# Optimization experiments

Hardware: AMD Instinct MI355X
Metric: run time of the kernel (lower is better)

Reference implementation:

```python
import jax, jax.numpy as jnp
import numpy as np

N = 8192; S = 32; EMB = 256; NH = 8; HD = EMB // NH; NT = 4; K = 2; L = 2; E = 131072
IN_DIMS = [128, 64, 32, 16]; COUNTS = [4096, 2048, 1024, 1024]
BETA = 1.0; TEMPER = 1.0; SLOPE = 0.2; LN_EPS = 1e-5


def setup_inputs() -> dict:
    key = jax.random.key(0)
    ks = iter(jax.random.split(key, 64))
    def nrm(shape, scale=1.0):
        return jax.random.normal(next(ks), shape, jnp.float32) * scale
    inp = {}
    for i, (d, c) in enumerate(zip(IN_DIMS, COUNTS)):
        inp[f"feat{i}"] = nrm((c, d))
        inp[f"Wfc{i}"] = nrm((d, EMB), d ** -0.5)
        inp[f"bfc{i}"] = nrm((EMB,), 0.01)
    inp["type_emb"] = nrm((NT, NT))
    inp["Wgcn"] = nrm((K, EMB, EMB), EMB ** -0.5)
    inp["bgcn"] = nrm((K, EMB), 0.01)
    inp["Wre"] = nrm((K, NT, NT), NT ** -0.5)
    inp["bre"] = nrm((K, NT), 0.01)
    inp["wtre"] = jnp.ones((K, NT), jnp.float32)
    inp["Wl"] = nrm((L, EMB, EMB), EMB ** -0.5)
    inp["Wr"] = nrm((L, EMB, EMB), EMB ** -0.5)
    inp["al"] = nrm((L, HD), HD ** -0.5)
    inp["ar"] = nrm((L, HD), HD ** -0.5)
    inp["Wrs"] = nrm((L, NT, NT * NH), NT ** -0.5)
    inp["Wrt"] = nrm((L, NT, NT * NH), NT ** -0.5)
    inp["Wfin"] = nrm((L, EMB, EMB), EMB ** -0.5)
    inp["ln_g"] = jnp.ones((L, EMB), jnp.float32)
    inp["ln_b"] = jnp.zeros((L, EMB), jnp.float32)
    inp["src"] = jax.random.randint(next(ks), (E,), 0, N)
    inp["dst"] = jax.random.randint(next(ks), (E,), 0, N)
    inp["node_type"] = jnp.concatenate([jnp.full((c,), t, jnp.int32) for t, c in enumerate(COUNTS)])
    inp["seqs"] = jax.random.randint(next(ks), (N, S), 0, N)
    return inp


def _l2n(x):
    return x / jnp.maximum(jnp.linalg.norm(x, axis=1, keepdims=True), 1e-12)


def _ln(x, g, b):
    m = x.mean(-1, keepdims=True)
    v = ((x - m) ** 2).mean(-1, keepdims=True)
    return (x - m) * jax.lax.rsqrt(v + LN_EPS) * g + b


def _agt(h, rh, Wl_, Wr_, al_, ar_, Wrs_, Wrt_, Wfin_, g_, b_):
    B, Sq, _ = h.shape
    fl = (h @ Wl_).reshape(B, Sq, NH, HD).transpose(0, 2, 1, 3)  # [B,NH,S,HD]
    fr = (h @ Wr_).reshape(B, Sq, NH, HD).transpose(0, 2, 1, 3)
    sl = jnp.einsum('bhsd,d->bhs', jax.nn.leaky_relu(fl, SLOPE), al_)
    sr = jnp.einsum('bhsd,d->bhs', jax.nn.leaky_relu(fr, SLOPE), ar_)
    score = sl[:, :, :, None] + sr[:, :, None, :]  # [B,NH,S,S]
    rk = (rh @ Wrs_).reshape(B, Sq, NH, NT).transpose(0, 2, 1, 3)  # [B,NH,S,NT]
    rq = (rh @ Wrt_).reshape(B, Sq, NH, NT).transpose(0, 2, 1, 3)
    score = score + BETA * jnp.einsum('bhir,bhjr->bhij', rk, rq)
    attn = jax.nn.softmax(score / TEMPER, axis=-1)
    ctx = jnp.einsum('bhij,bhjd->bhid', attn, fr)
    h_sa = ctx.transpose(0, 2, 1, 3).reshape(B, Sq, EMB)
    return _ln(h + h_sa @ Wfin_, g_, b_)


def reference(feat0, feat1, feat2, feat3, Wfc0, bfc0, Wfc1, bfc1, Wfc2, bfc2, Wfc3, bfc3,
              type_emb, Wgcn, bgcn, Wre, bre, wtre, Wl, Wr, al, ar, Wrs, Wrt, Wfin, ln_g, ln_b,
              src, dst, node_type, seqs):
    feats = [feat0, feat1, feat2, feat3]
    Wfcs = [Wfc0, Wfc1, Wfc2, Wfc3]
    bfcs = [bfc0, bfc1, bfc2, bfc3]
    gh = jnp.concatenate([f @ W + b for f, W, b in zip(feats, Wfcs, bfcs)], axis=0)  # [N,EMB]
    Nn = gh.shape[0]
    loop = jnp.arange(Nn, dtype=src.dtype)  # self-loops (graph.add_self_loop)
    src_f = jnp.concatenate([src, loop]); dst_f = jnp.concatenate([dst, loop])
    ones = jnp.ones(src_f.shape[0], jnp.float32)
    outdeg = jnp.clip(jax.ops.segment_sum(ones, src_f, num_segments=Nn), 1.0)
    indeg = jnp.clip(jax.ops.segment_sum(ones, dst_f, num_segments=Nn), 1.0)
    n_out = outdeg ** -0.5; n_in = indeg ** -0.5
    ret = [_l2n(gh)]
    R = type_emb[node_type]  # [N,NT]
    for k in range(K):
        # GraphConv, norm='both', relu
        x = (gh * n_out[:, None]) @ Wgcn[k]
        gh = jax.nn.relu(jax.ops.segment_sum(x[src_f], dst_f, num_segments=Nn) * n_in[:, None] + bgcn[k])
        # REConv: left norm, weight, per-node type scale, scatter-sum, right norm, bias, relu
        r = ((R * n_out[:, None]) @ Wre[k]) * wtre[k][node_type][:, None]
        R = jax.nn.relu(jax.ops.segment_sum(r[src_f], dst_f, num_segments=Nn) * n_in[:, None] + bre[k])
    h = gh[seqs]   # [N,S,EMB]
    rh = R[seqs]   # [N,S,NT]
    for l in range(L):
        h = _agt(h, rh, Wl[l], Wr[l], al[l], ar[l], Wrs[l], Wrt[l], Wfin[l], ln_g[l], ln_b[l])
        ret.append(_l2n(h[:, 0, :]))
    return jnp.concatenate(ret, axis=1)  # [N, EMB*(1+L)]
```

## Files before the change

kernel.cpp:

```cpp
#include <hip/hip_runtime.h>
#include <hip/hip_bf16.h>
#include <cstdint>
#include <cstddef>

typedef unsigned short ushortT;
typedef unsigned int uintT;

using bf16x8 = __attribute__((ext_vector_type(8))) short;
using f32x4  = __attribute__((ext_vector_type(4))) float;

static constexpr int NN  = 8192;
static constexpr int EE  = 131072;
static constexpr float SLOPE  = 0.2f;
static constexpr float LN_EPS = 1e-5f;

#define DEVI __device__ __forceinline__

DEVI float red32(float v) {
  #pragma unroll
  for (int m = 16; m >= 1; m >>= 1) v += __shfl_xor(v, m, 64);
  return v;
}
DEVI float red64(float v) {
  #pragma unroll
  for (int m = 32; m >= 1; m >>= 1) v += __shfl_xor(v, m, 64);
  return v;
}
DEVI float max32(float v) {
  #pragma unroll
  for (int m = 16; m >= 1; m >>= 1) v = fmaxf(v, __shfl_xor(v, m, 64));
  return v;
}
DEVI float blo(uintT u) { union { uintT i; float f; } c; c.i = u << 16; return c.f; }
DEVI float bhi(uintT u) { union { uintT i; float f; } c; c.i = u & 0xffff0000u; return c.f; }
DEVI float b2f(ushortT u) { union { uintT i; float f; } c; c.i = ((uintT)u) << 16; return c.f; }
DEVI ushortT f2bu(float f) {
  __hip_bfloat16 h = __float2bfloat16(f);
  return *reinterpret_cast<ushortT*>(&h);
}
DEVI void storeC(float* p, float v) { *p = v; }
DEVI void storeC(ushortT* p, float v) { *p = f2bu(v); }

__global__ __launch_bounds__(256) void fc_kernel(
    const float* __restrict__ f0, const float* __restrict__ f1,
    const float* __restrict__ f2, const float* __restrict__ f3,
    const float* __restrict__ w0, const float* __restrict__ w1,
    const float* __restrict__ w2, const float* __restrict__ w3,
    const float* __restrict__ b0, const float* __restrict__ b1,
    const float* __restrict__ b2, const float* __restrict__ b3,
    float* __restrict__ gh, float* __restrict__ out)
{
  const int nb = blockIdx.x * 32;
  const int t  = threadIdx.x;
  int base, D;
  const float *F, *W, *Bv;
  if (nb < 4096)      { base = 0;    D = 128; F = f0; W = w0; Bv = b0; }
  else if (nb < 6144) { base = 4096; D = 64;  F = f1; W = w1; Bv = b1; }
  else if (nb < 7168) { base = 6144; D = 32;  F = f2; W = w2; Bv = b2; }
  else                { base = 7168; D = 16;  F = f3; W = w3; Bv = b3; }

  __shared__ float Fs[32 * 128];
  __shared__ float red[32][4];
  __shared__ float nrm[32];

  const int total = 32 * D;
  for (int i = t; i < total; i += 256) Fs[i] = F[(size_t)(nb - base) * D + i];
  __syncthreads();

  float acc[32];
  #pragma unroll
  for (int r = 0; r < 32; ++r) acc[r] = Bv[t];
  for (int d = 0; d < D; ++d) {
    float w = W[(size_t)d * 256 + t];
    #pragma unroll
    for (int r = 0; r < 32; ++r) acc[r] = fmaf(Fs[r * D + d], w, acc[r]);
  }

  const int lane = t & 63, wid = t >> 6;
  #pragma unroll
  for (int r = 0; r < 32; ++r) {
    float v = acc[r] * acc[r];
    for (int o = 32; o > 0; o >>= 1) v += __shfl_down(v, o, 64);
    if (lane == 0) red[r][wid] = v;
  }
  __syncthreads();
  if (t < 32) {
    float s = red[t][0] + red[t][1] + red[t][2] + red[t][3];
    nrm[t] = 1.0f / fmaxf(sqrtf(s), 1e-12f);
  }
  __syncthreads();
  #pragma unroll
  for (int r = 0; r < 32; ++r) {
    gh[(size_t)(nb + r) * 256 + t]  = acc[r];
    out[(size_t)(nb + r) * 768 + t] = acc[r] * nrm[r];
  }
}

__global__ __launch_bounds__(256) void zero_counts(int* outc, int* inc) {
  int g = blockIdx.x * 256 + threadIdx.x;
  if (g < NN) outc[g] = 0; else inc[g - NN] = 0;
}
__global__ __launch_bounds__(256) void count_deg(const int* __restrict__ src,
                                                 const int* __restrict__ dst,
                                                 int* outc, int* inc) {
  int g = blockIdx.x * 256 + threadIdx.x;
  atomicAdd(&outc[src[g]], 1);
  atomicAdd(&inc[dst[g]], 1);
}
__global__ __launch_bounds__(1024) void scan_kernel(
    const int* __restrict__ inc, const int* __restrict__ outc,
    int* __restrict__ offs, int* __restrict__ cur,
    float* __restrict__ n_out, float* __restrict__ n_in)
{
  __shared__ int sums[1024];
  const int t = threadIdx.x;
  int x[8];
  const int base = t * 8;
  int s = 0;
  #pragma unroll
  for (int i = 0; i < 8; ++i) { int v = inc[base + i] + 1; x[i] = s; s += v; }
  sums[t] = s;
  __syncthreads();
  for (int off = 1; off < 1024; off <<= 1) {
    int a = (t >= off) ? sums[t - off] : 0;
    __syncthreads();
    sums[t] += a;
    __syncthreads();
  }
  const int pre = (t > 0) ? sums[t - 1] : 0;
  #pragma unroll
  for (int i = 0; i < 8; ++i) {
    const int o = pre + x[i];
    offs[base + i] = o;
    cur[base + i]  = o;
    n_in[base + i]  = rsqrtf((float)inc[base + i] + 1.0f);
    n_out[base + i] = rsqrtf((float)outc[base + i] + 1.0f);
  }
  if (t == 1023) offs[NN] = sums[1023];
}
__global__ __launch_bounds__(256) void fill_csr(const int* __restrict__ src,
                                                const int* __restrict__ dst,
                                                int* cur, int* __restrict__ csr) {
  int g = blockIdx.x * 256 + threadIdx.x;
  int s, d;
  if (g < EE) { s = src[g]; d = dst[g]; }
  else        { s = g - EE; d = g - EE; }
  int pos = atomicAdd(&cur[d], 1);
  csr[pos] = s;
}
__global__ __launch_bounds__(256) void init_R(const float* __restrict__ type_emb,
                                              const int* __restrict__ nt,
                                              float* __restrict__ R) {
  int g = blockIdx.x * 256 + threadIdx.x;
  int n = g >> 2, c = g & 3;
  R[g] = type_emb[nt[n] * 4 + c];
}

template<bool ROWSCALE, bool STORE, bool RED, typename CT>
__global__ __launch_bounds__(256) void mfma_gemm_kernel(
    const float* __restrict__ A, const float* __restrict__ W,
    const float* __restrict__ rowscale,
    CT* __restrict__ C, const float* __restrict__ avec,
    float* __restrict__ SSo)
{
  const int m0 = blockIdx.x * 64;
  const int n0 = blockIdx.y * 64;
  const int t = threadIdx.x;
  const int w = t >> 6, l = t & 63;
  const int wr = w >> 1, wc = w & 1;
  const int l15 = l & 15, l16 = l >> 4;

  __shared__ alignas(16) ushortT As[64][72];
  __shared__ alignas(16) ushortT Bs[64][72];

  f32x4 acc[2][2];
  #pragma unroll
  for (int mh = 0; mh < 2; ++mh)
    #pragma unroll
    for (int nh = 0; nh < 2; ++nh)
      #pragma unroll
      for (int r = 0; r < 4; ++r) acc[mh][nh][r] = 0.f;

  for (int k0 = 0; k0 < 256; k0 += 64) {
    #pragma unroll
    for (int rep = 0; rep < 16; ++rep) {
      int flat = rep * 256 + t;
      int r = flat >> 6, k = flat & 63;
      float v = A[(size_t)(m0 + r) * 256 + k0 + k];
      if constexpr (ROWSCALE) v *= rowscale[m0 + r];
      As[r][k] = f2bu(v);
    }
    #pragma unroll
    for (int rep = 0; rep < 16; ++rep) {
      int flat = rep * 256 + t;
      int k = flat >> 6, n = flat & 63;
      Bs[n][k] = f2bu(W[(size_t)(k0 + k) * 256 + n0 + n]);
    }
    __syncthreads();
    #pragma unroll
    for (int ks = 0; ks < 2; ++ks) {
      const int kb = ks * 32 + l16 * 8;
      bf16x8 afr[2], bfr[2];
      #pragma unroll
      for (int mh = 0; mh < 2; ++mh)
        afr[mh] = *reinterpret_cast<const bf16x8*>(&As[wr * 32 + mh * 16 + l15][kb]);
      #pragma unroll
      for (int nh = 0; nh < 2; ++nh)
        bfr[nh] = *reinterpret_cast<const bf16x8*>(&Bs[wc * 32 + nh * 16 + l15][kb]);
      #pragma unroll
      for (int mh = 0; mh < 2; ++mh)
        #pragma unroll
        for (int nh = 0; nh < 2; ++nh)
          acc[mh][nh] = __builtin_amdgcn_mfma_f32_16x16x32_bf16(
              afr[mh], bfr[nh], acc[mh][nh], 0, 0, 0);
    }
    __syncthreads();
  }
  if constexpr (STORE) {
    #pragma unroll
    for (int mh = 0; mh < 2; ++mh)
      #pragma unroll
      for (int nh = 0; nh < 2; ++nh)
        #pragma unroll
        for (int r = 0; r < 4; ++r) {
          const int row = m0 + wr * 32 + mh * 16 + l16 * 4 + r;
          const int col = n0 + wc * 32 + nh * 16 + l15;
          storeC(&C[(size_t)row * 256 + col], acc[mh][nh][r]);
        }
  }
  if constexpr (RED) {
    const float av0 = avec[l15], av1 = avec[16 + l15];
    #pragma unroll
    for (int mh = 0; mh < 2; ++mh)
      #pragma unroll
      for (int r = 0; r < 4; ++r) {
        float s = 0.f;
        {
          float x = acc[mh][0][r];
          s = fmaf(x > 0.f ? x : SLOPE * x, av0, s);
          x = acc[mh][1][r];
          s = fmaf(x > 0.f ? x : SLOPE * x, av1, s);
        }
        #pragma unroll
        for (int m = 8; m >= 1; m >>= 1) s += __shfl_xor(s, m, 64);
        if (l15 == 0) {
          const int row = m0 + wr * 32 + mh * 16 + l16 * 4 + r;
          SSo[(size_t)row * 8 + blockIdx.y * 2 + wc] = s;
        }
      }
  }
}

__global__ __launch_bounds__(256) void mfma_wlwr_kernel(
    const float* __restrict__ A,
    const float* __restrict__ Wl_, const float* __restrict__ Wr_,
    float* __restrict__ GR1,
    const float* __restrict__ al_, const float* __restrict__ ar_,
    float* __restrict__ SL, float* __restrict__ SR)
{
  const int m0 = blockIdx.x * 64;
  const int n0 = blockIdx.y * 64;
  const int t = threadIdx.x;
  const int w = t >> 6, l = t & 63;
  const int wr = w >> 1, wc = w & 1;
  const int l15 = l & 15, l16 = l >> 4;

  __shared__ alignas(16) ushortT As[64][72];
  __shared__ alignas(16) ushortT Bl[64][72];
  __shared__ alignas(16) ushortT Br[64][72];

  f32x4 accl[2][2], accr[2][2];
  #pragma unroll
  for (int mh = 0; mh < 2; ++mh)
    #pragma unroll
    for (int nh = 0; nh < 2; ++nh)
      #pragma unroll
      for (int r = 0; r < 4; ++r) { accl[mh][nh][r] = 0.f; accr[mh][nh][r] = 0.f; }

  for (int k0 = 0; k0 < 256; k0 += 64) {
    #pragma unroll
    for (int rep = 0; rep < 16; ++rep) {
      int flat = rep * 256 + t;
      int r = flat >> 6, k = flat & 63;
      As[r][k] = f2bu(A[(size_t)(m0 + r) * 256 + k0 + k]);
    }
    #pragma unroll
    for (int rep = 0; rep < 16; ++rep) {
      int flat = rep * 256 + t;
      int k = flat >> 6, n = flat & 63;
      Bl[n][k] = f2bu(Wl_[(size_t)(k0 + k) * 256 + n0 + n]);
      Br[n][k] = f2bu(Wr_[(size_t)(k0 + k) * 256 + n0 + n]);
    }
    __syncthreads();
    #pragma unroll
    for (int ks = 0; ks < 2; ++ks) {
      const int kb = ks * 32 + l16 * 8;
      bf16x8 afr[2], blr[2], brr[2];
      #pragma unroll
      for (int mh = 0; mh < 2; ++mh)
        afr[mh] = *reinterpret_cast<const bf16x8*>(&As[wr * 32 + mh * 16 + l15][kb]);
      #pragma unroll
      for (int nh = 0; nh < 2; ++nh) {
        blr[nh] = *reinterpret_cast<const bf16x8*>(&Bl[wc * 32 + nh * 16 + l15][kb]);
        brr[nh] = *reinterpret_cast<const bf16x8*>(&Br[wc * 32 + nh * 16 + l15][kb]);
      }
      #pragma unroll
      for (int mh = 0; mh < 2; ++mh)
        #pragma unroll
        for (int nh = 0; nh < 2; ++nh) {
          accl[mh][nh] = __builtin_amdgcn_mfma_f32_16x16x32_bf16(
              afr[mh], blr[nh], accl[mh][nh], 0, 0, 0);
          accr[mh][nh] = __builtin_amdgcn_mfma_f32_16x16x32_bf16(
              afr[mh], brr[nh], accr[mh][nh], 0, 0, 0);
        }
    }
    __syncthreads();
  }
  #pragma unroll
  for (int mh = 0; mh < 2; ++mh)
    #pragma unroll
    for (int nh = 0; nh < 2; ++nh)
      #pragma unroll
      for (int r = 0; r < 4; ++r) {
        const int row = m0 + wr * 32 + mh * 16 + l16 * 4 + r;
        const int col = n0 + wc * 32 + nh * 16 + l15;
        GR1[(size_t)row * 256 + col] = accr[mh][nh][r];
      }
  const float al0 = al_[l15], al1 = al_[16 + l15];
  const float ar0 = ar_[l15], ar1 = ar_[16 + l15];
  #pragma unroll
  for (int mh = 0; mh < 2; ++mh)
    #pragma unroll
    for (int r = 0; r < 4; ++r) {
      float sl = 0.f, sr = 0.f;
      {
        float x = accl[mh][0][r];
        sl = fmaf(x > 0.f ? x : SLOPE * x, al0, sl);
        x = accl[mh][1][r];
        sl = fmaf(x > 0.f ? x : SLOPE * x, al1, sl);
        x = accr[mh][0][r];
        sr = fmaf(x > 0.f ? x : SLOPE * x, ar0, sr);
        x = accr[mh][1][r];
        sr = fmaf(x > 0.f ? x : SLOPE * x, ar1, sr);
      }
      #pragma unroll
      for (int m = 8; m >= 1; m >>= 1) {
        sl += __shfl_xor(sl, m, 64);
        sr += __shfl_xor(sr, m, 64);
      }
      if (l15 == 0) {
        const int row = m0 + wr * 32 + mh * 16 + l16 * 4 + r;
        SL[(size_t)row * 8 + blockIdx.y * 2 + wc] = sl;
        SR[(size_t)row * 8 + blockIdx.y * 2 + wc] = sr;
      }
    }
}

__global__ __launch_bounds__(256) void agg2_kernel(
    const int* __restrict__ offs, const int* __restrict__ csr,
    const ushortT* __restrict__ X, const float* __restrict__ n_in,
    const float* __restrict__ bias, float* __restrict__ ghn,
    ushortT* __restrict__ ghb)
{
  const int n  = blockIdx.x * 2 + (threadIdx.x >> 7);
  const int tc = threadIdx.x & 127;
  const uintT* X2 = reinterpret_cast<const uintT*>(X);
  const int s0 = offs[n], s1 = offs[n + 1];
  float a0 = 0.f, a1 = 0.f;
  for (int i = s0; i < s1; ++i) {
    const uintT u = X2[(size_t)csr[i] * 128 + tc];
    a0 += blo(u);
    a1 += bhi(u);
  }
  const float ni = n_in[n];
  const float g0 = fmaxf(fmaf(a0, ni, bias[2 * tc]), 0.f);
  const float g1 = fmaxf(fmaf(a1, ni, bias[2 * tc + 1]), 0.f);
  float2 g2; g2.x = g0; g2.y = g1;
  reinterpret_cast<float2*>(ghn)[(size_t)n * 128 + tc] = g2;
  if (ghb)
    reinterpret_cast<uintT*>(ghb)[(size_t)n * 128 + tc] =
        (uintT)f2bu(g0) | ((uintT)f2bu(g1) << 16);
}

__global__ __launch_bounds__(256) void re_proj(
    const float* __restrict__ R, const float* __restrict__ n_out,
    const float* __restrict__ Wre, const float* __restrict__ wtre,
    const int* __restrict__ nt, float* __restrict__ rtmp)
{
  int g = blockIdx.x * 256 + threadIdx.x;
  int n = g >> 2, j = g & 3;
  float s = 0.f;
  #pragma unroll
  for (int c = 0; c < 4; ++c) s += R[n * 4 + c] * Wre[c * 4 + j];
  rtmp[g] = s * n_out[n] * wtre[nt[n]];
}
__global__ __launch_bounds__(256) void re_agg(
    const int* __restrict__ offs, const int* __restrict__ csr,
    const float* __restrict__ rtmp, const float* __restrict__ n_in,
    const float* __restrict__ bre, float* __restrict__ Rn)
{
  int g = blockIdx.x * 256 + threadIdx.x;
  int n = g >> 2, j = g & 3;
  float a = 0.f;
  for (int i = offs[n]; i < offs[n + 1]; ++i) a += rtmp[csr[i] * 4 + j];
  Rn[g] = fmaxf(fmaf(a, n_in[n], bre[j]), 0.f);
}
__global__ __launch_bounds__(256) void rkq_kernel(
    const float* __restrict__ R, const float* __restrict__ Wrs,
    const float* __restrict__ Wrt, float* __restrict__ RKQ)
{
  int g = blockIdx.x * 256 + threadIdx.x;
  int n = g >> 7, c = g & 127;
  int which = c >> 5, cc = c & 31;
  const float* Wp = (which == 0) ? Wrs : (which == 1) ? Wrt
                   : (which == 2) ? (Wrs + 128) : (Wrt + 128);
  float s = 0.f;
  #pragma unroll
  for (int r = 0; r < 4; ++r) s += R[n * 4 + r] * Wp[r * 32 + cc];
  RKQ[g] = s;
}

__global__ __launch_bounds__(256) void vec4_kernel(
    const float* __restrict__ ln_g, const float* __restrict__ ln_b,
    const float* __restrict__ Wr2, float* __restrict__ vecs)
{
  const int which = blockIdx.x, t = threadIdx.x;
  const float* s = (which & 1) ? ln_b : ln_g;
  float a = 0.f;
  for (int k = 0; k < 256; ++k) a = fmaf(s[k], Wr2[(size_t)k * 256 + t], a);
  vecs[which * 256 + t] = a;
}
__global__ __launch_bounds__(256) void wg2i_kernel(
    const float* __restrict__ ln_g, const float* __restrict__ Wr2,
    ushortT* __restrict__ Wg2i)
{
  const int gid = blockIdx.x * 256 + threadIdx.x;
  const int ks  = gid >> 10;
  const int cgl = (gid >> 6) & 15;
  const int l   = gid & 63;
  const int col = cgl * 16 + (l & 15);
  const int kb  = ks * 32 + (l >> 4) * 8;
  ushortT v[8];
  #pragma unroll
  for (int e = 0; e < 8; ++e)
    v[e] = f2bu(ln_g[kb + e] * Wr2[(size_t)(kb + e) * 256 + col]);
  *reinterpret_cast<bf16x8*>(&Wg2i[(size_t)gid * 8]) =
      *reinterpret_cast<const bf16x8*>(v);
}
__global__ __launch_bounds__(256) void wcvt_kernel(
    const float* __restrict__ Wl2, const float* __restrict__ Wfin2,
    ushortT* __restrict__ Wl2b, ushortT* __restrict__ Wf2b)
{
  int g = blockIdx.x * 256 + threadIdx.x;
  if (g < 65536) Wl2b[g] = f2bu(Wl2[g]);
  else { int q = g - 65536; Wf2b[q] = f2bu(Wfin2[q]); }
}

__global__ __launch_bounds__(256) void mega8_kernel(
    const int* __restrict__ seqs,
    const ushortT* __restrict__ ghb,
    const ushortT* __restrict__ GW,
    const float* __restrict__ SLg, const float* __restrict__ SRg,
    const float* __restrict__ RKQ,
    const float* __restrict__ vecs,
    const ushortT* __restrict__ Wg2i,
    const ushortT* __restrict__ Wl2b,
    const ushortT* __restrict__ Wf2b,
    const float* __restrict__ al2, const float* __restrict__ ar2,
    const float* __restrict__ ln_g, const float* __restrict__ ln_b,
    float* __restrict__ out)
{
  __shared__ int idx[32];
  __shared__ alignas(16) ushortT bufA[10240];
  __shared__ alignas(16) ushortT bufB[10240];
  __shared__ float SRs[8][32];
  __shared__ float RQs[32][36];
  __shared__ float rk2s[32];
  __shared__ float part[32][4], partq[32][4];
  __shared__ float mu_s[32], rs_s[32];
  __shared__ float SR2s[8][32];
  __shared__ float sl2s[8];
  __shared__ float scp[8][32];
  __shared__ float h1r0s[256];
  __shared__ float ctx2s[256];
  __shared__ float wred4[4];
  __shared__ float nrm1s;

  const int b = blockIdx.x, t = threadIdx.x;
  const int h8 = t >> 5, lo = t & 31;
  const int w = t >> 6, l = t & 63;
  const int l15 = l & 15, l16 = l >> 4;

  if (t < 32) idx[t] = seqs[b * 32 + t];
  __syncthreads();

  const float sli = SLg[(size_t)idx[lo] * 8 + h8];
  const float rk0 = RKQ[(size_t)idx[lo] * 128 + h8 * 4 + 0];
  const float rk1 = RKQ[(size_t)idx[lo] * 128 + h8 * 4 + 1];
  const float rk2_ = RKQ[(size_t)idx[lo] * 128 + h8 * 4 + 2];
  const float rk3 = RKQ[(size_t)idx[lo] * 128 + h8 * 4 + 3];

  {
    const uintT* GWu = reinterpret_cast<const uintT*>(GW);
    #pragma unroll
    for (int rep = 0; rep < 16; ++rep) {
      int flat = rep * 256 + t;
      int j = flat >> 7, cp = flat & 127;
      const uintT u = GWu[(size_t)idx[j] * 128 + cp];
      const int rA = 2 * cp;
      const int k = (rA >> 3) & 3;
      const int off = (((j >> 3) ^ k) << 3) + (j & 7);
      bufA[rA * 40 + off]       = (ushortT)(u & 0xffffu);
      bufA[(rA + 1) * 40 + off] = (ushortT)(u >> 16);
    }
  }
  SRs[h8][lo] = SRg[(size_t)idx[lo] * 8 + h8];
  #pragma unroll
  for (int rep = 0; rep < 4; ++rep) {
    int flat = rep * 256 + t, s3 = flat >> 5, c3 = flat & 31;
    RQs[s3][c3] = RKQ[(size_t)idx[s3] * 128 + 32 + c3];
  }
  if (t < 32) rk2s[t] = RKQ[(size_t)idx[0] * 128 + 64 + t];
  __syncthreads();

  {
    float p1[32];
    float m = -1e30f;
    #pragma unroll
    for (int j = 0; j < 32; ++j) {
      float sc = sli + SRs[h8][j]
               + rk0 * RQs[j][h8 * 4 + 0] + rk1 * RQs[j][h8 * 4 + 1]
               + rk2_ * RQs[j][h8 * 4 + 2] + rk3 * RQs[j][h8 * 4 + 3];
      p1[j] = sc; m = fmaxf(m, sc);
    }
    float sum = 0.f;
    #pragma unroll
    for (int j = 0; j < 32; ++j) { p1[j] = __expf(p1[j] - m); sum += p1[j]; }
    const float inv = 1.f / sum;
    const int row = t;
    const int k = (row >> 3) & 3;
    uintT* pw = reinterpret_cast<uintT*>(bufB) + row * 20;
    #pragma unroll
    for (int o = 0; o < 4; ++o) {
      uint4 v;
      v.x = (uintT)f2bu(p1[8 * o + 0] * inv) | ((uintT)f2bu(p1[8 * o + 1] * inv) << 16);
      v.y = (uintT)f2bu(p1[8 * o + 2] * inv) | ((uintT)f2bu(p1[8 * o + 3] * inv) << 16);
      v.z = (uintT)f2bu(p1[8 * o + 4] * inv) | ((uintT)f2bu(p1[8 * o + 5] * inv) << 16);
      v.w = (uintT)f2bu(p1[8 * o + 6] * inv) | ((uintT)f2bu(p1[8 * o + 7] * inv) << 16);
      *reinterpret_cast<uint4*>(pw + ((o ^ k) << 2)) = v;
    }
  }
  __syncthreads();

  int irow[2][4];
  #pragma unroll
  for (int mh = 0; mh < 2; ++mh)
    #pragma unroll
    for (int r = 0; r < 4; ++r)
      irow[mh][r] = idx[mh * 16 + l16 * 4 + r];

  bf16x8 af[2][2];
  #pragma unroll
  for (int hh = 0; hh < 2; ++hh) {
    const int h = 2 * w + hh;
    #pragma unroll
    for (int mh = 0; mh < 2; ++mh) {
      const int row = h * 32 + mh * 16 + l15;
      const int k = (row >> 3) & 3;
      af[hh][mh] = *reinterpret_cast<const bf16x8*>(&bufB[row * 40 + ((l16 ^ k) << 3)]);
    }
  }

  f32x4 acc[2][2][2];
  #pragma unroll
  for (int hh = 0; hh < 2; ++hh) {
    const int h = 2 * w + hh;
    bf16x8 bf[2];
    #pragma unroll
    for (int nh = 0; nh < 2; ++nh) {
      const int row = h * 32 + nh * 16 + l15;
      const int k = (row >> 3) & 3;
      bf[nh] = *reinterpret_cast<const bf16x8*>(&bufA[row * 40 + ((l16 ^ k) << 3)]);
    }
    #pragma unroll
    for (int mh = 0; mh < 2; ++mh)
      #pragma unroll
      for (int nh = 0; nh < 2; ++nh) {
        f32x4 z = {0.f, 0.f, 0.f, 0.f};
        acc[hh][mh][nh] = __builtin_amdgcn_mfma_f32_16x16x32_bf16(af[hh][mh], bf[nh], z, 0, 0, 0);
      }
  }
  {
    float sum_[2][4], sq_[2][4];
    #pragma unroll
    for (int mh = 0; mh < 2; ++mh)
      #pragma unroll
      for (int r = 0; r < 4; ++r) { sum_[mh][r] = 0.f; sq_[mh][r] = 0.f; }
    #pragma unroll
    for (int hh = 0; hh < 2; ++hh)
      #pragma unroll
      for (int mh = 0; mh < 2; ++mh)
        #pragma unroll
        for (int nh = 0; nh < 2; ++nh) {
          const int col = (2 * w + hh) * 32 + nh * 16 + l15;
          #pragma unroll
          for (int r = 0; r < 4; ++r) {
            float v = acc[hh][mh][nh][r] + b2f(ghb[(size_t)irow[mh][r] * 256 + col]);
            acc[hh][mh][nh][r] = v;
            sum_[mh][r] += v;
            sq_[mh][r] = fmaf(v, v, sq_[mh][r]);
          }
        }
    #pragma unroll
    for (int mh = 0; mh < 2; ++mh)
      #pragma unroll
      for (int r = 0; r < 4; ++r) {
        float s = sum_[mh][r], q = sq_[mh][r];
        #pragma unroll
        for (int m = 8; m >= 1; m >>= 1) {
          s += __shfl_xor(s, m, 64);
          q += __shfl_xor(q, m, 64);
        }
        if (l15 == 0) {
          part[mh * 16 + l16 * 4 + r][w]  = s;
          partq[mh * 16 + l16 * 4 + r][w] = q;
        }
      }
    if (l16 == 0) {
      #pragma unroll
      for (int hh = 0; hh < 2; ++hh)
        #pragma unroll
        for (int nh = 0; nh < 2; ++nh)
          h1r0s[(2 * w + hh) * 32 + nh * 16 + l15] = acc[hh][0][nh][0];
    }
  }
  __syncthreads();

  if (t < 32) {
    float sm = part[t][0] + part[t][1] + part[t][2] + part[t][3];
    float sq = partq[t][0] + partq[t][1] + partq[t][2] + partq[t][3];
    const float m = sm * (1.f / 256.f);
    const float v = fmaxf(sq * (1.f / 256.f) - m * m, 0.f);
    mu_s[t] = m;
    rs_s[t] = rsqrtf(v + LN_EPS);
  }
  __syncthreads();

  #pragma unroll
  for (int hh = 0; hh < 2; ++hh)
    #pragma unroll
    for (int mh = 0; mh < 2; ++mh)
      #pragma unroll
      for (int nh = 0; nh < 2; ++nh) {
        const int col = (2 * w + hh) * 32 + nh * 16 + l15;
        #pragma unroll
        for (int r = 0; r < 4; ++r) {
          const int row = mh * 16 + l16 * 4 + r;
          bufB[row * 264 + col] = f2bu(acc[hh][mh][nh][r]);
        }
      }
  #pragma unroll
  for (int rep = 0; rep < 4; ++rep) {
    int flat = rep * 256 + t, s3 = flat >> 5, c3 = flat & 31;
    RQs[s3][c3] = RKQ[(size_t)idx[s3] * 128 + 96 + c3];
  }
  {
    const float mu0 = mu_s[0], rs0 = rs_s[0];
    float hv = fmaf((h1r0s[t] - mu0) * rs0, ln_g[t], ln_b[t]);
    float sq = red64(hv * hv);
    h1r0s[t] = hv;
    if ((t & 63) == 0) wred4[t >> 6] = sq;
  }
  __syncthreads();

  if (t == 0) nrm1s = 1.f / fmaxf(sqrtf(wred4[0] + wred4[1] + wred4[2] + wred4[3]), 1e-12f);

  {
    f32x4 acc2[2][4];
    #pragma unroll
    for (int mh = 0; mh < 2; ++mh)
      #pragma unroll
      for (int cg = 0; cg < 4; ++cg)
        #pragma unroll
        for (int r = 0; r < 4; ++r) acc2[mh][cg][r] = 0.f;
    #pragma unroll
    for (int ks = 0; ks < 8; ++ks) {
      const int ko = ks * 32 + l16 * 8;
      bf16x8 a2[2];
      #pragma unroll
      for (int mh = 0; mh < 2; ++mh)
        a2[mh] = *reinterpret_cast<const bf16x8*>(&bufB[(mh * 16 + l15) * 264 + ko]);
      #pragma unroll
      for (int cg = 0; cg < 4; ++cg) {
        const bf16x8 b2 = *reinterpret_cast<const bf16x8*>(
            &Wg2i[((size_t)(ks * 16 + (w * 4 + cg)) * 64 + l) * 8]);
        #pragma unroll
        for (int mh = 0; mh < 2; ++mh)
          acc2[mh][cg] = __builtin_amdgcn_mfma_f32_16x16x32_bf16(a2[mh], b2, acc2[mh][cg], 0, 0, 0);
      }
    }
    float rsv[2][4], rmv[2][4];
    #pragma unroll
    for (int mh = 0; mh < 2; ++mh)
      #pragma unroll
      for (int r = 0; r < 4; ++r) {
        const int row = mh * 16 + l16 * 4 + r;
        rsv[mh][r] = rs_s[row];
        rmv[mh][r] = rsv[mh][r] * mu_s[row];
      }
    float sacc[2][2][4];
    #pragma unroll
    for (int hh = 0; hh < 2; ++hh)
      #pragma unroll
      for (int mh = 0; mh < 2; ++mh)
        #pragma unroll
        for (int r = 0; r < 4; ++r) sacc[hh][mh][r] = 0.f;
    float ar2v[2] = { ar2[l15], ar2[16 + l15] };
    #pragma unroll
    for (int cg = 0; cg < 4; ++cg) {
      const int col = w * 64 + cg * 16 + l15;
      const float v1c = vecs[col], v2c = vecs[256 + col];
      const int hh = cg >> 1;
      #pragma unroll
      for (int mh = 0; mh < 2; ++mh)
        #pragma unroll
        for (int r = 0; r < 4; ++r) {
          const int row = mh * 16 + l16 * 4 + r;
          float fa = fmaf(rsv[mh][r], acc2[mh][cg][r], fmaf(-rmv[mh][r], v1c, v2c));
          bufA[row * 268 + col] = f2bu(fa);
          float lr = fa > 0.f ? fa : SLOPE * fa;
          sacc[hh][mh][r] = fmaf(lr, ar2v[cg & 1], sacc[hh][mh][r]);
        }
    }
    #pragma unroll
    for (int hh = 0; hh < 2; ++hh)
      #pragma unroll
      for (int mh = 0; mh < 2; ++mh)
        #pragma unroll
        for (int r = 0; r < 4; ++r) {
          float s = sacc[hh][mh][r];
          #pragma unroll
          for (int m = 8; m >= 1; m >>= 1) s += __shfl_xor(s, m, 64);
          if (l15 == 0) SR2s[2 * w + hh][mh * 16 + l16 * 4 + r] = s;
        }
  }
  {
    float fl = 0.f;
    #pragma unroll 8
    for (int k = 0; k < 256; ++k)
      fl = fmaf(h1r0s[k], b2f(Wl2b[(size_t)k * 256 + t]), fl);
    float lr = (fl > 0.f ? fl : SLOPE * fl) * al2[lo];
    lr = red32(lr);
    if (lo == 0) sl2s[h8] = lr;
  }
  __syncthreads();

  {
    float s2 = sl2s[h8] + SR2s[h8][lo]
             + rk2s[h8 * 4 + 0] * RQs[lo][h8 * 4 + 0]
             + rk2s[h8 * 4 + 1] * RQs[lo][h8 * 4 + 1]
             + rk2s[h8 * 4 + 2] * RQs[lo][h8 * 4 + 2]
             + rk2s[h8 * 4 + 3] * RQs[lo][h8 * 4 + 3];
    const float m2 = max32(s2);
    const float e = __expf(s2 - m2);
    const float su = red32(e);
    scp[h8][lo] = e / su;
  }
  __syncthreads();

  {
    float a = 0.f;
    #pragma unroll
    for (int j = 0; j < 32; ++j) a = fmaf(scp[h8][j], b2f(bufA[j * 268 + t]), a);
    ctx2s[t] = a;
  }
  out[(size_t)b * 768 + 256 + t] = h1r0s[t] * nrm1s;
  __syncthreads();

  {
    float yv = 0.f;
    #pragma unroll 8
    for (int k = 0; k < 256; ++k)
      yv = fmaf(ctx2s[k], b2f(Wf2b[(size_t)k * 256 + t]), yv);
    const float y = yv + h1r0s[t];
    float s = red64(y);
    float q = red64(y * y);
    if ((t & 63) == 0) { part[0][t >> 6] = s; partq[0][t >> 6] = q; }
    __syncthreads();
    const float mu = (part[0][0] + part[0][1] + part[0][2] + part[0][3]) * (1.f / 256.f);
    const float var = fmaxf((partq[0][0] + partq[0][1] + partq[0][2] + partq[0][3]) * (1.f / 256.f) - mu * mu, 0.f);
    const float rstd = rsqrtf(var + LN_EPS);
    const float yn = fmaf((y - mu) * rstd, ln_g[256 + t], ln_b[256 + t]);
    float nq = red64(yn * yn);
    if ((t & 63) == 0) part[1][t >> 6] = nq;
    __syncthreads();
    const float nrm = 1.f / fmaxf(sqrtf(part[1][0] + part[1][1] + part[1][2] + part[1][3]), 1e-12f);
    out[(size_t)b * 768 + 512 + t] = yn * nrm;
  }
}

extern "C" void kernel_launch(void* const* d_in, const int* in_sizes, int n_in,
                              void* d_out, int out_size, void* d_ws, size_t ws_size,
                              hipStream_t stream)
{
  (void)in_sizes; (void)n_in; (void)out_size; (void)ws_size;

  const float* feat[4]; const float* wfc[4]; const float* bfc[4];
  for (int i = 0; i < 4; ++i) {
    feat[i] = (const float*)d_in[i * 3 + 0];
    wfc[i]  = (const float*)d_in[i * 3 + 1];
    bfc[i]  = (const float*)d_in[i * 3 + 2];
  }
  const float* type_emb = (const float*)d_in[12];
  const float* Wgcn = (const float*)d_in[13];
  const float* bgcn = (const float*)d_in[14];
  const float* Wre  = (const float*)d_in[15];
  const float* bre  = (const float*)d_in[16];
  const float* wtre = (const float*)d_in[17];
  const float* Wl   = (const float*)d_in[18];
  const float* Wr   = (const float*)d_in[19];
  const float* al   = (const float*)d_in[20];
  const float* ar   = (const float*)d_in[21];
  const float* Wrs  = (const float*)d_in[22];
  const float* Wrt  = (const float*)d_in[23];
  const float* Wfin = (const float*)d_in[24];
  const float* ln_g = (const float*)d_in[25];
  const float* ln_b = (const float*)d_in[26];
  const int* src       = (const int*)d_in[27];
  const int* dst       = (const int*)d_in[28];
  const int* node_type = (const int*)d_in[29];
  const int* seqs      = (const int*)d_in[30];
  float* out = (float*)d_out;

  char* p = (char*)d_ws;
  auto take = [&](size_t n) { char* q = p; p += (n + 255) & ~(size_t)255; return q; };
  float* gh    = (float*)take((size_t)NN * 256 * 4);
  float* GR1   = (float*)take((size_t)NN * 256 * 4);
  float* RKQ   = (float*)take((size_t)NN * 128 * 4);
  float* SLg   = (float*)take((size_t)NN * 8 * 4);
  float* SRg   = (float*)take((size_t)NN * 8 * 4);
  float* n_out = (float*)take((size_t)NN * 4);
  float* n_in_ = (float*)take((size_t)NN * 4);
  int*   outc  = (int*)take((size_t)NN * 4);
  int*   inc   = (int*)take((size_t)NN * 4);
  int*   offs  = (int*)take((size_t)(NN + 1) * 4);
  int*   cur   = (int*)take((size_t)NN * 4);
  int*   csr   = (int*)take((size_t)(EE + NN) * 4);
  float* R     = (float*)take((size_t)NN * 4 * 4);
  float* rtmp  = (float*)take((size_t)NN * 4 * 4);
  ushortT* GW   = (ushortT*)take((size_t)NN * 256 * 2);
  ushortT* ghb  = (ushortT*)take((size_t)NN * 256 * 2);
  ushortT* Xb   = (ushortT*)take((size_t)NN * 256 * 2);
  ushortT* Wg2i = (ushortT*)take((size_t)131072 * 2);
  ushortT* Wl2b = (ushortT*)take((size_t)65536 * 2);
  ushortT* Wf2b = (ushortT*)take((size_t)65536 * 2);
  float* vecs  = (float*)take((size_t)2 * 256 * 4);

  const float* Wr2 = Wr + 65536;
  const float* Wl2 = Wl + 65536;

  fc_kernel<<<256, 256, 0, stream>>>(feat[0], feat[1], feat[2], feat[3],
                                     wfc[0], wfc[1], wfc[2], wfc[3],
                                     bfc[0], bfc[1], bfc[2], bfc[3], gh, out);
  zero_counts<<<64, 256, 0, stream>>>(outc, inc);
  count_deg<<<512, 256, 0, stream>>>(src, dst, outc, inc);
  scan_kernel<<<1, 1024, 0, stream>>>(inc, outc, offs, cur, n_out, n_in_);
  fill_csr<<<544, 256, 0, stream>>>(src, dst, cur, csr);
  init_R<<<128, 256, 0, stream>>>(type_emb, node_type, R);

  vec4_kernel<<<2, 256, 0, stream>>>(ln_g, ln_b, Wr2, vecs);
  wg2i_kernel<<<64, 256, 0, stream>>>(ln_g, Wr2, Wg2i);
  wcvt_kernel<<<512, 256, 0, stream>>>(Wl2, Wfin + 65536, Wl2b, Wf2b);

  for (int k = 0; k < 2; ++k) {
    mfma_gemm_kernel<true, true, false, ushortT>
        <<<dim3(128, 4), 256, 0, stream>>>(gh, Wgcn + (size_t)k * 65536,
                                           n_out, Xb, nullptr, nullptr);
    agg2_kernel<<<NN / 2, 256, 0, stream>>>(offs, csr, Xb, n_in_,
                                            bgcn + k * 256, gh,
                                            k == 1 ? ghb : nullptr);
    re_proj<<<128, 256, 0, stream>>>(R, n_out, Wre + k * 16, wtre + k * 4, node_type, rtmp);
    re_agg<<<128, 256, 0, stream>>>(offs, csr, rtmp, n_in_, bre + k * 4, R);
  }

  rkq_kernel<<<4096, 256, 0, stream>>>(R, Wrs, Wrt, RKQ);
  mfma_wlwr_kernel<<<dim3(128, 4), 256, 0, stream>>>(
      gh, Wl, Wr, GR1, al, ar, SLg, SRg);
  mfma_gemm_kernel<false, true, false, ushortT>
      <<<dim3(128, 4), 256, 0, stream>>>(GR1, Wfin, nullptr, GW, nullptr, nullptr);

  mega8_kernel<<<NN, 256, 0, stream>>>(seqs, ghb, GW, SLg, SRg, RKQ, vecs,
                                       Wg2i, Wl2b, Wf2b,
                                       al + 32, ar + 32, ln_g, ln_b, out);
}
```

Baseline: 601.1 us.

## Move final Wfin projection out of mega kernel into batched MFMA GEMM

The per-row 256x256 Wfin matvec at the end of the mega kernel is removed. Each row's ctx2 and residual vectors are written to global buffers, then a batched MFMA GEMM over all 8192 rows and a separate LayerNorm plus L2-normalise kernel finish the computation. This replaces a scalar per-block matvec that rereads the full bf16 weight for every row with a tensor-core GEMM that reuses the weight. The cost is two extra launches and extra global traffic for the intermediates. The Wfin multiply now runs through the GEMM path on fp32 inputs, so its numeric precision may differ from the old bf16 weights.

```diff
diff --git a/kernel.cpp b/kernel.cpp
--- a/kernel.cpp
+++ b/kernel.cpp
@@ -447,16 +447,14 @@
   *reinterpret_cast<bf16x8*>(&Wg2i[(size_t)gid * 8]) =
       *reinterpret_cast<const bf16x8*>(v);
 }
-__global__ __launch_bounds__(256) void wcvt_kernel(
-    const float* __restrict__ Wl2, const float* __restrict__ Wfin2,
-    ushortT* __restrict__ Wl2b, ushortT* __restrict__ Wf2b)
+__global__ __launch_bounds__(256) void wl2b_kernel(
+    const float* __restrict__ Wl2, ushortT* __restrict__ Wl2b)
 {
   int g = blockIdx.x * 256 + threadIdx.x;
-  if (g < 65536) Wl2b[g] = f2bu(Wl2[g]);
-  else { int q = g - 65536; Wf2b[q] = f2bu(Wfin2[q]); }
-}
-
-__global__ __launch_bounds__(256) void mega8_kernel(
+  Wl2b[g] = f2bu(Wl2[g]);
+}
+
+__global__ __launch_bounds__(256) void mega7_kernel(
     const int* __restrict__ seqs,
     const ushortT* __restrict__ ghb,
     const ushortT* __restrict__ GW,
@@ -465,9 +463,9 @@
     const float* __restrict__ vecs,
     const ushortT* __restrict__ Wg2i,
     const ushortT* __restrict__ Wl2b,
-    const ushortT* __restrict__ Wf2b,
     const float* __restrict__ al2, const float* __restrict__ ar2,
     const float* __restrict__ ln_g, const float* __restrict__ ln_b,
+    float* __restrict__ h1r0buf, float* __restrict__ ctx2buf,
     float* __restrict__ out)
 {
   __shared__ int idx[32];
@@ -482,7 +480,6 @@
   __shared__ float sl2s[8];
   __shared__ float scp[8][32];
   __shared__ float h1r0s[256];
-  __shared__ float ctx2s[256];
   __shared__ float wred4[4];
   __shared__ float nrm1s;
 
@@ -667,6 +664,7 @@
   {
     const float mu0 = mu_s[0], rs0 = rs_s[0];
     float hv = fmaf((h1r0s[t] - mu0) * rs0, ln_g[t], ln_b[t]);
+    h1r0buf[(size_t)b * 256 + t] = hv;
     float sq = red64(hv * hv);
     h1r0s[t] = hv;
     if ((t & 63) == 0) wred4[t >> 6] = sq;
@@ -772,31 +770,33 @@
     float a = 0.f;
     #pragma unroll
     for (int j = 0; j < 32; ++j) a = fmaf(scp[h8][j], b2f(bufA[j * 268 + t]), a);
-    ctx2s[t] = a;
+    ctx2buf[(size_t)b * 256 + t] = a;
   }
   out[(size_t)b * 768 + 256 + t] = h1r0s[t] * nrm1s;
-  __syncthreads();
-
-  {
-    float yv = 0.f;
-    #pragma unroll 8
-    for (int k = 0; k < 256; ++k)
-      yv = fmaf(ctx2s[k], b2f(Wf2b[(size_t)k * 256 + t]), yv);
-    const float y = yv + h1r0s[t];
-    float s = red64(y);
-    float q = red64(y * y);
-    if ((t & 63) == 0) { part[0][t >> 6] = s; partq[0][t >> 6] = q; }
-    __syncthreads();
-    const float mu = (part[0][0] + part[0][1] + part[0][2] + part[0][3]) * (1.f / 256.f);
-    const float var = fmaxf((partq[0][0] + partq[0][1] + partq[0][2] + partq[0][3]) * (1.f / 256.f) - mu * mu, 0.f);
-    const float rstd = rsqrtf(var + LN_EPS);
-    const float yn = fmaf((y - mu) * rstd, ln_g[256 + t], ln_b[256 + t]);
-    float nq = red64(yn * yn);
-    if ((t & 63) == 0) part[1][t >> 6] = nq;
-    __syncthreads();
-    const float nrm = 1.f / fmaxf(sqrtf(part[1][0] + part[1][1] + part[1][2] + part[1][3]), 1e-12f);
-    out[(size_t)b * 768 + 512 + t] = yn * nrm;
-  }
+}
+
+__global__ __launch_bounds__(256) void ln_l2n_kernel(
+    const float* __restrict__ Y, const float* __restrict__ res,
+    const float* __restrict__ lng, const float* __restrict__ lnb,
+    float* __restrict__ out)
+{
+  const int row = blockIdx.x, t = threadIdx.x;
+  __shared__ float s4[4], q4[4];
+  const float y = Y[(size_t)row * 256 + t] + res[(size_t)row * 256 + t];
+  float s = red64(y);
+  float q = red64(y * y);
+  if ((t & 63) == 0) { s4[t >> 6] = s; q4[t >> 6] = q; }
+  __syncthreads();
+  const float mu = (s4[0] + s4[1] + s4[2] + s4[3]) * (1.f / 256.f);
+  const float var = fmaxf((q4[0] + q4[1] + q4[2] + q4[3]) * (1.f / 256.f) - mu * mu, 0.f);
+  const float rstd = rsqrtf(var + LN_EPS);
+  const float yn = fmaf((y - mu) * rstd, lng[t], lnb[t]);
+  float nq = red64(yn * yn);
+  __syncthreads();
+  if ((t & 63) == 0) s4[t >> 6] = nq;
+  __syncthreads();
+  const float nrm = 1.f / fmaxf(sqrtf(s4[0] + s4[1] + s4[2] + s4[3]), 1e-12f);
+  out[(size_t)row * 768 + 512 + t] = yn * nrm;
 }
 
 extern "C" void kernel_launch(void* const* d_in, const int* in_sizes, int n_in,
@@ -835,6 +835,7 @@
   char* p = (char*)d_ws;
   auto take = [&](size_t n) { char* q = p; p += (n + 255) & ~(size_t)255; return q; };
   float* gh    = (float*)take((size_t)NN * 256 * 4);
+  float* Xf    = (float*)take((size_t)NN * 256 * 4);
   float* GR1   = (float*)take((size_t)NN * 256 * 4);
   float* RKQ   = (float*)take((size_t)NN * 128 * 4);
   float* SLg   = (float*)take((size_t)NN * 8 * 4);
@@ -853,8 +854,10 @@
   ushortT* Xb   = (ushortT*)take((size_t)NN * 256 * 2);
   ushortT* Wg2i = (ushortT*)take((size_t)131072 * 2);
   ushortT* Wl2b = (ushortT*)take((size_t)65536 * 2);
-  ushortT* Wf2b = (ushortT*)take((size_t)65536 * 2);
   float* vecs  = (float*)take((size_t)2 * 256 * 4);
+  float* ctx2buf = Xf;
+  float* h1r0buf = GR1;
+  float* Yb      = gh;
 
   const float* Wr2 = Wr + 65536;
   const float* Wl2 = Wl + 65536;
@@ -870,7 +873,7 @@
 
   vec4_kernel<<<2, 256, 0, stream>>>(ln_g, ln_b, Wr2, vecs);
   wg2i_kernel<<<64, 256, 0, stream>>>(ln_g, Wr2, Wg2i);
-  wcvt_kernel<<<512, 256, 0, stream>>>(Wl2, Wfin + 65536, Wl2b, Wf2b);
+  wl2b_kernel<<<256, 256, 0, stream>>>(Wl2, Wl2b);
 
   for (int k = 0; k < 2; ++k) {
     mfma_gemm_kernel<true, true, false, ushortT>
@@ -889,7 +892,13 @@
   mfma_gemm_kernel<false, true, false, ushortT>
       <<<dim3(128, 4), 256, 0, stream>>>(GR1, Wfin, nullptr, GW, nullptr, nullptr);
 
-  mega8_kernel<<<NN, 256, 0, stream>>>(seqs, ghb, GW, SLg, SRg, RKQ, vecs,
-                                       Wg2i, Wl2b, Wf2b,
-                                       al + 32, ar + 32, ln_g, ln_b, out);
-}
+  mega7_kernel<<<NN, 256, 0, stream>>>(seqs, ghb, GW, SLg, SRg, RKQ, vecs,
+                                       Wg2i, Wl2b,
+                                       al + 32, ar + 32, ln_g, ln_b,
+                                       h1r0buf, ctx2buf, out);
+
+  mfma_gemm_kernel<false, true, false, float>
+      <<<dim3(128, 4), 256, 0, stream>>>(ctx2buf, Wfin + 65536, nullptr,
+                                         Yb, nullptr, nullptr);
+  ln_l2n_kernel<<<NN, 256, 0, stream>>>(Yb, h1r0buf, ln_g + 256, ln_b + 256, out);
+}
```

Result: faster. 527.4 us (-12.3%).
